# Performance work log

Measured on AMD Instinct MI355X. Metric: run time of the kernel, lower is better.

The kernel has to match this reference:

```python
import jax, jax.numpy as jnp
import numpy as np

V = 50000
E = 10000
Q = 32
F_DIM = 256
OUT_DIM = 256
B = 2


def setup_inputs() -> dict:
    key = jax.random.key(0)
    k1, k2, k3, k4 = jax.random.split(key, 4)
    X = jax.random.normal(k1, (B, V, F_DIM), dtype=jnp.float32)
    edge_nodes = jax.random.randint(k2, (E, Q), 0, V, dtype=jnp.int64)
    W = jax.random.normal(k3, (OUT_DIM, F_DIM), dtype=jnp.float32) * (1.0 / np.sqrt(F_DIM))
    b = jax.random.normal(k4, (OUT_DIM,), dtype=jnp.float32) * 0.01
    return {"X": X, "edge_nodes": edge_nodes, "W": W, "b": b}


def reference(X, edge_nodes, W, b):
    # X: [B, V, F]; edge_nodes: [E, Q] node indices per hyperedge
    Bn, Vn, Fn = X.shape
    En, Qn = edge_nodes.shape
    # gather-mean per hyperedge: agg[b,e,:] = mean_q X[b, edge_nodes[e,q], :]
    gathered = X[:, edge_nodes, :]                      # [B, E, Q, F]
    agg = gathered.mean(axis=2)                          # [B, E, F]
    flat = edge_nodes.reshape(-1)                        # [E*Q]
    # scatter-add agg back to every member node of its hyperedge
    vals = jnp.broadcast_to(agg[:, :, None, :], (Bn, En, Qn, Fn)).reshape(Bn, En * Qn, Fn)
    X_out = jnp.zeros_like(X).at[:, flat, :].add(vals)   # [B, V, F]
    # degree = number of hyperedge memberships per node, clamped to >= 1
    deg = jnp.zeros((Vn,), X.dtype).at[flat].add(1.0)
    deg = jnp.maximum(deg, 1.0)
    X_out = X_out / deg[None, :, None]
    # fc: Linear(in_dim, out_dim)
    return X_out @ W.T + b
```

## Files before the change

kernel.cpp:

```cpp
#include <hip/hip_runtime.h>
#include <hip/hip_bf16.h>
#include <stdint.h>

static constexpr int V_N = 50000;
static constexpr int E_N = 10000;
static constexpr int Q_N = 32;
static constexpr int F_N = 256;
static constexpr int M_N = 2 * E_N;
static constexpr int SLOT_STRIDE = 40;

typedef unsigned short us;
typedef float f32x4 __attribute__((ext_vector_type(4)));
typedef us us4 __attribute__((ext_vector_type(4)));
typedef __bf16 bf16x8 __attribute__((ext_vector_type(8)));

__device__ __forceinline__ us f2b(float f) {
  unsigned x = __builtin_bit_cast(unsigned, f);
  x += 0x7fffu + ((x >> 16) & 1u);
  return (us)(x >> 16);
}
__device__ __forceinline__ float b2f(us u) {
  unsigned x = ((unsigned)u) << 16;
  return __builtin_bit_cast(float, x);
}


static constexpr int NXV = (2 * V_N * F_N) / 4;
static constexpr int NWV = (F_N * F_N) / 4;

__global__ __launch_bounds__(256) void k_prep(const float* __restrict__ X,
                                              const float* __restrict__ Wm,
                                              us* __restrict__ Xb,
                                              us* __restrict__ Wb) {
  int i = blockIdx.x * 256 + threadIdx.x;
  if (i < NXV) {
    f32x4 v = ((const f32x4*)X)[i];
    us4 o;
    #pragma unroll
    for (int j = 0; j < 4; ++j) o[j] = f2b(v[j]);
    ((us4*)Xb)[i] = o;
  } else if (i < NXV + NWV) {
    int k = i - NXV;
    f32x4 v = ((const f32x4*)Wm)[k];
    us4 o;
    #pragma unroll
    for (int j = 0; j < 4; ++j) o[j] = f2b(v[j]);
    ((us4*)Wb)[k] = o;
  }
}


__global__ void k_bucket(const int* __restrict__ en, int* __restrict__ cnt,
                         int* __restrict__ slots) {
  int i = blockIdx.x * 256 + threadIdx.x;
  if (i >= E_N * Q_N) return;
  int v = en[i];
  int pos = atomicAdd(&cnt[v], 1);
  if (pos < SLOT_STRIDE) slots[v * SLOT_STRIDE + pos] = i >> 5;
}


__global__ __launch_bounds__(256) void k_agg(const us* __restrict__ Xb,
                                             const int* __restrict__ en,
                                             us* __restrict__ agg) {
  int wv = threadIdx.x >> 6;
  int lane = threadIdx.x & 63;
  int e = blockIdx.x * 4 + wv;
  int myn = en[e * Q_N + (lane & 31)];
  int col = lane * 4;
  const us* X0 = Xb + col;
  const us* X1 = Xb + (size_t)V_N * F_N + col;
  float a0[4] = {0, 0, 0, 0}, a1[4] = {0, 0, 0, 0};
  #pragma unroll 4
  for (int q = 0; q < Q_N; ++q) {
    int n = __shfl(myn, q, 64);
    size_t off = (size_t)n * F_N;
    us4 u0 = *(const us4*)(X0 + off);
    us4 u1 = *(const us4*)(X1 + off);
    #pragma unroll
    for (int j = 0; j < 4; ++j) { a0[j] += b2f(u0[j]); a1[j] += b2f(u1[j]); }
  }
  const float s = 1.0f / 32.0f;
  us4 o0, o1;
  #pragma unroll
  for (int j = 0; j < 4; ++j) { o0[j] = f2b(a0[j] * s); o1[j] = f2b(a1[j] * s); }
  *(us4*)(agg + (size_t)e * F_N + col) = o0;
  *(us4*)(agg + (size_t)(E_N + e) * F_N + col) = o1;
}


__global__ __launch_bounds__(256) void k_gemm(const us* __restrict__ agg,
                                              const us* __restrict__ Wb,
                                              us* __restrict__ Yb) {
  int wave = (blockIdx.x * 256 + threadIdx.x) >> 6;
  int lane = threadIdx.x & 63;
  int mt = wave >> 4;
  int nt = wave & 15;
  int m = lane & 15;
  int quad = lane >> 4;
  const us* ap = agg + (size_t)(mt * 16 + m) * F_N + quad * 8;
  const us* bp = Wb + (size_t)(nt * 16 + m) * F_N + quad * 8;
  f32x4 acc = {0.f, 0.f, 0.f, 0.f};
  #pragma unroll
  for (int kk = 0; kk < 8; ++kk) {
    bf16x8 a = *(const bf16x8*)(ap + kk * 32);
    bf16x8 bv = *(const bf16x8*)(bp + kk * 32);
    acc = __builtin_amdgcn_mfma_f32_16x16x32_bf16(a, bv, acc, 0, 0, 0);
  }
  us* yp = Yb + (size_t)(mt * 16 + quad * 4) * 256 + nt * 16 + m;
  #pragma unroll
  for (int r = 0; r < 4; ++r) yp[(size_t)r * 256] = f2b(acc[r]);
}


__global__ __launch_bounds__(256) void k_out(const us* __restrict__ Yb,
                                             const int* __restrict__ cnt,
                                             const int* __restrict__ slots,
                                             const float* __restrict__ bias,
                                             float* __restrict__ out) {
  int wv = threadIdx.x >> 6;
  int lane = threadIdx.x & 63;
  int v = blockIdx.x * 4 + wv;
  int col = lane * 4;
  int c = cnt[v];
  if (c > SLOT_STRIDE) c = SLOT_STRIDE;
  const int* sb = slots + (size_t)v * SLOT_STRIDE;
  const us* Y0 = Yb + col;
  const us* Y1 = Yb + (size_t)E_N * 256 + col;
  float acc0[4] = {0, 0, 0, 0}, acc1[4] = {0, 0, 0, 0};
  int j = 0;
  for (; j + 2 <= c; j += 2) {
    int e0 = sb[j], e1 = sb[j + 1];
    us4 p00 = *(const us4*)(Y0 + (size_t)e0 * 256);
    us4 p01 = *(const us4*)(Y1 + (size_t)e0 * 256);
    us4 p10 = *(const us4*)(Y0 + (size_t)e1 * 256);
    us4 p11 = *(const us4*)(Y1 + (size_t)e1 * 256);
    #pragma unroll
    for (int k = 0; k < 4; ++k) {
      acc0[k] += b2f(p00[k]) + b2f(p10[k]);
      acc1[k] += b2f(p01[k]) + b2f(p11[k]);
    }
  }
  if (j < c) {
    int e0 = sb[j];
    us4 p00 = *(const us4*)(Y0 + (size_t)e0 * 256);
    us4 p01 = *(const us4*)(Y1 + (size_t)e0 * 256);
    #pragma unroll
    for (int k = 0; k < 4; ++k) { acc0[k] += b2f(p00[k]); acc1[k] += b2f(p01[k]); }
  }
  float inv = 1.0f / (float)(c > 0 ? c : 1);
  f32x4 bb = *(const f32x4*)(bias + col);
  f32x4 r0, r1;
  #pragma unroll
  for (int k = 0; k < 4; ++k) {
    r0[k] = bb[k] + acc0[k] * inv;
    r1[k] = bb[k] + acc1[k] * inv;
  }
  *(f32x4*)(out + (size_t)v * 256 + col) = r0;
  *(f32x4*)(out + ((size_t)V_N + v) * 256 + col) = r1;
}


extern "C" void kernel_launch(void* const* d_in, const int* in_sizes, int n_in,
                              void* d_out, int out_size, void* d_ws, size_t ws_size,
                              hipStream_t stream) {
  (void)in_sizes; (void)n_in; (void)out_size; (void)ws_size;
  const float* X = (const float*)d_in[0];
  const int* en = (const int*)d_in[1];
  const float* Wm = (const float*)d_in[2];
  const float* bias = (const float*)d_in[3];
  float* out = (float*)d_out;

  char* ws = (char*)d_ws;
  int* cnt   = (int*)(ws);
  int* slots = (int*)(ws + (1u << 20));
  us*  Wb    = (us*)(ws + (10u << 20));
  us*  agg   = (us*)(ws + (11u << 20));
  us*  Yb    = (us*)(ws + (22u << 20));
  us*  Xb    = (us*)(ws + (33u << 20));

  hipMemsetAsync(cnt, 0, V_N * sizeof(int), stream);
  k_prep<<<(NXV + NWV + 255) / 256, 256, 0, stream>>>(X, Wm, Xb, Wb);
  k_bucket<<<(E_N * Q_N + 255) / 256, 256, 0, stream>>>(en, cnt, slots);
  k_agg<<<E_N / 4, 256, 0, stream>>>(Xb, en, agg);
  k_gemm<<<M_N / 4, 256, 0, stream>>>(agg, Wb, Yb);
  k_out<<<V_N / 4, 256, 0, stream>>>(Yb, cnt, slots, bias, out);
}
```

Baseline: 327.8 us.

## Fuse prep with bucketing and aggregation with GEMM via LDS tile

Merges the bf16 conversion and the node-to-hyperedge bucketing into one grid-stride kernel. Fuses the per-hyperedge gather-mean with the MFMA GEMM: each block aggregates 8 hyperedges for both batches into an LDS tile, then multiplies against W without writing agg to global memory. The output scatter loop is unrolled by four for more memory-level parallelism. This removes two launches and the agg round trip. In exchange, W is re-read by every block, and the GEMM tiles cover only 8 real rows per batch, so MFMA work per block is lower.

```diff
diff --git a/kernel.cpp b/kernel.cpp
--- a/kernel.cpp
+++ b/kernel.cpp
@@ -6,8 +6,12 @@
 static constexpr int E_N = 10000;
 static constexpr int Q_N = 32;
 static constexpr int F_N = 256;
-static constexpr int M_N = 2 * E_N;
 static constexpr int SLOT_STRIDE = 40;
+static constexpr int NXV = (2 * V_N * F_N) / 4;
+static constexpr int NWV = (F_N * F_N) / 4;
+static constexpr int T_TILES = E_N / 8;
+static constexpr int LDS_STRIDE = 264;
+static constexpr int PREP_GRID = 2048;
 
 typedef unsigned short us;
 typedef float f32x4 __attribute__((ext_vector_type(4)));
@@ -25,102 +29,113 @@
 }
 
 
-static constexpr int NXV = (2 * V_N * F_N) / 4;
-static constexpr int NWV = (F_N * F_N) / 4;
-
-__global__ __launch_bounds__(256) void k_prep(const float* __restrict__ X,
-                                              const float* __restrict__ Wm,
-                                              us* __restrict__ Xb,
-                                              us* __restrict__ Wb) {
-  int i = blockIdx.x * 256 + threadIdx.x;
-  if (i < NXV) {
-    f32x4 v = ((const f32x4*)X)[i];
-    us4 o;
-    #pragma unroll
-    for (int j = 0; j < 4; ++j) o[j] = f2b(v[j]);
-    ((us4*)Xb)[i] = o;
-  } else if (i < NXV + NWV) {
-    int k = i - NXV;
-    f32x4 v = ((const f32x4*)Wm)[k];
-    us4 o;
-    #pragma unroll
-    for (int j = 0; j < 4; ++j) o[j] = f2b(v[j]);
-    ((us4*)Wb)[k] = o;
-  }
-}
-
-
-__global__ void k_bucket(const int* __restrict__ en, int* __restrict__ cnt,
-                         int* __restrict__ slots) {
-  int i = blockIdx.x * 256 + threadIdx.x;
-  if (i >= E_N * Q_N) return;
-  int v = en[i];
-  int pos = atomicAdd(&cnt[v], 1);
-  if (pos < SLOT_STRIDE) slots[v * SLOT_STRIDE + pos] = i >> 5;
-}
-
-
-__global__ __launch_bounds__(256) void k_agg(const us* __restrict__ Xb,
-                                             const int* __restrict__ en,
-                                             us* __restrict__ agg) {
-  int wv = threadIdx.x >> 6;
-  int lane = threadIdx.x & 63;
-  int e = blockIdx.x * 4 + wv;
-  int myn = en[e * Q_N + (lane & 31)];
-  int col = lane * 4;
+__global__ __launch_bounds__(256) void k_prep_bucket(
+    const float* __restrict__ X, const float* __restrict__ Wm,
+    const int* __restrict__ en, us* __restrict__ Xb, us* __restrict__ Wb,
+    int* __restrict__ cnt, int* __restrict__ slots) {
+  int tid = blockIdx.x * 256 + threadIdx.x;
+  const int NT = PREP_GRID * 256;
+  for (int i = tid; i < NXV + NWV; i += NT) {
+    if (i < NXV) {
+      f32x4 v = ((const f32x4*)X)[i];
+      us4 o;
+      #pragma unroll
+      for (int j = 0; j < 4; ++j) o[j] = f2b(v[j]);
+      ((us4*)Xb)[i] = o;
+    } else {
+      int k = i - NXV;
+      f32x4 v = ((const f32x4*)Wm)[k];
+      us4 o;
+      #pragma unroll
+      for (int j = 0; j < 4; ++j) o[j] = f2b(v[j]);
+      ((us4*)Wb)[k] = o;
+    }
+  }
+  for (int i = tid; i < E_N * Q_N; i += NT) {
+    int v = en[i];
+    int pos = atomicAdd(&cnt[v], 1);
+    if (pos < SLOT_STRIDE) slots[v * SLOT_STRIDE + pos] = i >> 5;
+  }
+}
+
+
+__global__ __launch_bounds__(256) void k_agg_gemm(
+    const us* __restrict__ Xb, const int* __restrict__ en,
+    const us* __restrict__ Wb, us* __restrict__ Yb) {
+  __shared__ us tile[16 * LDS_STRIDE];
+  const int t = blockIdx.x;
+  const int w = threadIdx.x >> 6;
+  const int lane = threadIdx.x & 63;
+  const int m = lane & 15;
+  const int quad = lane >> 4;
+  const int col = lane * 4;
+
+  int e0 = t * 8 + 2 * w;
+  int n0 = en[e0 * Q_N + (lane & 31)];
+  int n1 = en[(e0 + 1) * Q_N + (lane & 31)];
   const us* X0 = Xb + col;
   const us* X1 = Xb + (size_t)V_N * F_N + col;
-  float a0[4] = {0, 0, 0, 0}, a1[4] = {0, 0, 0, 0};
+  float a00[4] = {0, 0, 0, 0}, a01[4] = {0, 0, 0, 0};
+  float a10[4] = {0, 0, 0, 0}, a11[4] = {0, 0, 0, 0};
   #pragma unroll 4
   for (int q = 0; q < Q_N; ++q) {
-    int n = __shfl(myn, q, 64);
-    size_t off = (size_t)n * F_N;
-    us4 u0 = *(const us4*)(X0 + off);
-    us4 u1 = *(const us4*)(X1 + off);
-    #pragma unroll
-    for (int j = 0; j < 4; ++j) { a0[j] += b2f(u0[j]); a1[j] += b2f(u1[j]); }
+    int ma = __shfl(n0, q, 64);
+    int mb = __shfl(n1, q, 64);
+    us4 u0a = *(const us4*)(X0 + (size_t)ma * F_N);
+    us4 u1a = *(const us4*)(X1 + (size_t)ma * F_N);
+    us4 u0b = *(const us4*)(X0 + (size_t)mb * F_N);
+    us4 u1b = *(const us4*)(X1 + (size_t)mb * F_N);
+    #pragma unroll
+    for (int j = 0; j < 4; ++j) {
+      a00[j] += b2f(u0a[j]); a01[j] += b2f(u1a[j]);
+      a10[j] += b2f(u0b[j]); a11[j] += b2f(u1b[j]);
+    }
   }
   const float s = 1.0f / 32.0f;
-  us4 o0, o1;
-  #pragma unroll
-  for (int j = 0; j < 4; ++j) { o0[j] = f2b(a0[j] * s); o1[j] = f2b(a1[j] * s); }
-  *(us4*)(agg + (size_t)e * F_N + col) = o0;
-  *(us4*)(agg + (size_t)(E_N + e) * F_N + col) = o1;
-}
-
-
-__global__ __launch_bounds__(256) void k_gemm(const us* __restrict__ agg,
-                                              const us* __restrict__ Wb,
-                                              us* __restrict__ Yb) {
-  int wave = (blockIdx.x * 256 + threadIdx.x) >> 6;
+  int s0 = 2 * w, s1 = 2 * w + 1;
+  us4 o0, o1, o2, o3;
+  #pragma unroll
+  for (int j = 0; j < 4; ++j) {
+    o0[j] = f2b(a00[j] * s); o1[j] = f2b(a01[j] * s);
+    o2[j] = f2b(a10[j] * s); o3[j] = f2b(a11[j] * s);
+  }
+  *(us4*)(tile + s0 * LDS_STRIDE + col) = o0;
+  *(us4*)(tile + (8 + s0) * LDS_STRIDE + col) = o1;
+  *(us4*)(tile + s1 * LDS_STRIDE + col) = o2;
+  *(us4*)(tile + (8 + s1) * LDS_STRIDE + col) = o3;
+  __syncthreads();
+
+  bf16x8 af[8];
+  #pragma unroll
+  for (int kk = 0; kk < 8; ++kk)
+    af[kk] = *(const bf16x8*)(tile + m * LDS_STRIDE + quad * 8 + kk * 32);
+  #pragma unroll
+  for (int i = 0; i < 4; ++i) {
+    int nt = w * 4 + i;
+    const us* bp = Wb + (size_t)(nt * 16 + m) * F_N + quad * 8;
+    f32x4 acc = {0.f, 0.f, 0.f, 0.f};
+    #pragma unroll
+    for (int kk = 0; kk < 8; ++kk) {
+      bf16x8 bv = *(const bf16x8*)(bp + kk * 32);
+      acc = __builtin_amdgcn_mfma_f32_16x16x32_bf16(af[kk], bv, acc, 0, 0, 0);
+    }
+    #pragma unroll
+    for (int r = 0; r < 4; ++r) {
+      int dr = quad * 4 + r;
+      int yrow = (dr < 8) ? (t * 8 + dr) : (E_N + t * 8 + dr - 8);
+      Yb[(size_t)yrow * 256 + nt * 16 + m] = f2b(acc[r]);
+    }
+  }
+}
+
+
+__global__ __launch_bounds__(256) void k_out(
+    const us* __restrict__ Yb, const int* __restrict__ cnt,
+    const int* __restrict__ slots, const float* __restrict__ bias,
+    float* __restrict__ out) {
+  int w = threadIdx.x >> 6;
   int lane = threadIdx.x & 63;
-  int mt = wave >> 4;
-  int nt = wave & 15;
-  int m = lane & 15;
-  int quad = lane >> 4;
-  const us* ap = agg + (size_t)(mt * 16 + m) * F_N + quad * 8;
-  const us* bp = Wb + (size_t)(nt * 16 + m) * F_N + quad * 8;
-  f32x4 acc = {0.f, 0.f, 0.f, 0.f};
-  #pragma unroll
-  for (int kk = 0; kk < 8; ++kk) {
-    bf16x8 a = *(const bf16x8*)(ap + kk * 32);
-    bf16x8 bv = *(const bf16x8*)(bp + kk * 32);
-    acc = __builtin_amdgcn_mfma_f32_16x16x32_bf16(a, bv, acc, 0, 0, 0);
-  }
-  us* yp = Yb + (size_t)(mt * 16 + quad * 4) * 256 + nt * 16 + m;
-  #pragma unroll
-  for (int r = 0; r < 4; ++r) yp[(size_t)r * 256] = f2b(acc[r]);
-}
-
-
-__global__ __launch_bounds__(256) void k_out(const us* __restrict__ Yb,
-                                             const int* __restrict__ cnt,
-                                             const int* __restrict__ slots,
-                                             const float* __restrict__ bias,
-                                             float* __restrict__ out) {
-  int wv = threadIdx.x >> 6;
-  int lane = threadIdx.x & 63;
-  int v = blockIdx.x * 4 + wv;
+  int v = blockIdx.x * 4 + w;
   int col = lane * 4;
   int c = cnt[v];
   if (c > SLOT_STRIDE) c = SLOT_STRIDE;
@@ -129,24 +144,28 @@
   const us* Y1 = Yb + (size_t)E_N * 256 + col;
   float acc0[4] = {0, 0, 0, 0}, acc1[4] = {0, 0, 0, 0};
   int j = 0;
-  for (; j + 2 <= c; j += 2) {
-    int e0 = sb[j], e1 = sb[j + 1];
-    us4 p00 = *(const us4*)(Y0 + (size_t)e0 * 256);
-    us4 p01 = *(const us4*)(Y1 + (size_t)e0 * 256);
-    us4 p10 = *(const us4*)(Y0 + (size_t)e1 * 256);
-    us4 p11 = *(const us4*)(Y1 + (size_t)e1 * 256);
+  for (; j + 4 <= c; j += 4) {
+    int ea = sb[j], eb = sb[j + 1], ec = sb[j + 2], ed = sb[j + 3];
+    us4 pa0 = *(const us4*)(Y0 + (size_t)ea * 256);
+    us4 pa1 = *(const us4*)(Y1 + (size_t)ea * 256);
+    us4 pb0 = *(const us4*)(Y0 + (size_t)eb * 256);
+    us4 pb1 = *(const us4*)(Y1 + (size_t)eb * 256);
+    us4 pc0 = *(const us4*)(Y0 + (size_t)ec * 256);
+    us4 pc1 = *(const us4*)(Y1 + (size_t)ec * 256);
+    us4 pd0 = *(const us4*)(Y0 + (size_t)ed * 256);
+    us4 pd1 = *(const us4*)(Y1 + (size_t)ed * 256);
     #pragma unroll
     for (int k = 0; k < 4; ++k) {
-      acc0[k] += b2f(p00[k]) + b2f(p10[k]);
-      acc1[k] += b2f(p01[k]) + b2f(p11[k]);
-    }
-  }
-  if (j < c) {
-    int e0 = sb[j];
-    us4 p00 = *(const us4*)(Y0 + (size_t)e0 * 256);
-    us4 p01 = *(const us4*)(Y1 + (size_t)e0 * 256);
-    #pragma unroll
-    for (int k = 0; k < 4; ++k) { acc0[k] += b2f(p00[k]); acc1[k] += b2f(p01[k]); }
+      acc0[k] += (b2f(pa0[k]) + b2f(pb0[k])) + (b2f(pc0[k]) + b2f(pd0[k]));
+      acc1[k] += (b2f(pa1[k]) + b2f(pb1[k])) + (b2f(pc1[k]) + b2f(pd1[k]));
+    }
+  }
+  for (; j < c; ++j) {
+    int e = sb[j];
+    us4 p0 = *(const us4*)(Y0 + (size_t)e * 256);
+    us4 p1 = *(const us4*)(Y1 + (size_t)e * 256);
+    #pragma unroll
+    for (int k = 0; k < 4; ++k) { acc0[k] += b2f(p0[k]); acc1[k] += b2f(p1[k]); }
   }
   float inv = 1.0f / (float)(c > 0 ? c : 1);
   f32x4 bb = *(const f32x4*)(bias + col);
@@ -175,14 +194,11 @@
   int* cnt   = (int*)(ws);
   int* slots = (int*)(ws + (1u << 20));
   us*  Wb    = (us*)(ws + (10u << 20));
-  us*  agg   = (us*)(ws + (11u << 20));
-  us*  Yb    = (us*)(ws + (22u << 20));
-  us*  Xb    = (us*)(ws + (33u << 20));
+  us*  Yb    = (us*)(ws + (11u << 20));
+  us*  Xb    = (us*)(ws + (22u << 20));
 
   hipMemsetAsync(cnt, 0, V_N * sizeof(int), stream);
-  k_prep<<<(NXV + NWV + 255) / 256, 256, 0, stream>>>(X, Wm, Xb, Wb);
-  k_bucket<<<(E_N * Q_N + 255) / 256, 256, 0, stream>>>(en, cnt, slots);
-  k_agg<<<E_N / 4, 256, 0, stream>>>(Xb, en, agg);
-  k_gemm<<<M_N / 4, 256, 0, stream>>>(agg, Wb, Yb);
+  k_prep_bucket<<<PREP_GRID, 256, 0, stream>>>(X, Wm, en, Xb, Wb, cnt, slots);
+  k_agg_gemm<<<T_TILES, 256, 0, stream>>>(Xb, en, Wb, Yb);
   k_out<<<V_N / 4, 256, 0, stream>>>(Yb, cnt, slots, bias, out);
 }
```

Measured after the change: 303.4 us. -7.5%, faster.
